# Kernel tuning notes

Measured on AMD Instinct MI355X. Metric: run time of the kernel, lower is better.

Reference implementation:

```python
import jax, jax.numpy as jnp
import numpy as np
from jax import lax

B, C, D, H, W = 2, 1, 128, 128, 128
CONSCIOUSNESS_WEIGHT = 0.1


def _field(depth, height, width, dtype):
    # sin(2*pi*(d+h+w)/(D+H+W)) broadcast over batch/channel
    d = jnp.arange(depth, dtype=dtype)[:, None, None]
    h = jnp.arange(height, dtype=dtype)[None, :, None]
    w = jnp.arange(width, dtype=dtype)[None, None, :]
    phase = 2.0 * jnp.pi * (d + h + w) / (depth + height + width)
    return jnp.sin(phase)  # [D,H,W]


def _conv3d(x, w, b):
    y = lax.conv_general_dilated(
        x, w, window_strides=(1, 1, 1), padding='SAME',
        dimension_numbers=('NCDHW', 'OIDHW', 'NCDHW'))
    return y + b[None, :, None, None, None]


def setup_inputs() -> dict:
    key = jax.random.key(0)
    ks = jax.random.split(key, 4)
    fan1 = 1 * 27
    fan2 = 8 * 27
    fan3 = 16 * 27
    return {
        'cube_data': jax.random.normal(ks[0], (B, C, D, H, W), dtype=jnp.float32),
        'w1': jax.random.normal(ks[1], (8, 1, 3, 3, 3), dtype=jnp.float32) / np.sqrt(fan1),
        'b1': jnp.zeros((8,), dtype=jnp.float32),
        'w2': jax.random.normal(ks[2], (16, 8, 3, 3, 3), dtype=jnp.float32) / np.sqrt(fan2),
        'b2': jnp.zeros((16,), dtype=jnp.float32),
        'w3': jax.random.normal(ks[3], (1, 16, 3, 3, 3), dtype=jnp.float32) / np.sqrt(fan3),
        'b3': jnp.zeros((1,), dtype=jnp.float32),
    }


def reference(cube_data, w1, b1, w2, b2, w3, b3):
    _, _, d, h, w = cube_data.shape
    field = _field(d, h, w, cube_data.dtype)[None, None]  # [1,1,D,H,W]
    integrated = cube_data * (1.0 + CONSCIOUSNESS_WEIGHT * field)
    x = jax.nn.relu(_conv3d(integrated, w1, b1))
    x = jax.nn.relu(_conv3d(x, w2, b2))
    x = jnp.tanh(_conv3d(x, w3, b3))
    return x
```

## Files before the change

### kernel.cpp

```cpp
#include <hip/hip_runtime.h>
#include <hip/hip_fp16.h>

#define VOX (128 * 128 * 128)
#define P 130
#define PP (P * P)
#define PVOX (P * P * P)
#define LROW 130
#define PLANE (6 * LROW)
#define C3PLANE 1560

typedef unsigned short u16;
typedef _Float16 f16x2 __attribute__((ext_vector_type(2)));
typedef _Float16 f16x8 __attribute__((ext_vector_type(8)));
typedef __attribute__((ext_vector_type(4))) float f32x4;

__device__ __forceinline__ u16 f2h(float f) {
    return __builtin_bit_cast(unsigned short, (_Float16)f);
}
__device__ __forceinline__ unsigned pkh_relu(float a, float b) {
    float ra = a > 0.f ? a : 0.f, rb = b > 0.f ? b : 0.f;
    return (unsigned)f2h(ra) | ((unsigned)f2h(rb) << 16);
}
__device__ __forceinline__ f16x2 h2(unsigned u) { return __builtin_bit_cast(f16x2, u); }

__device__ __forceinline__ float dot2(unsigned a, unsigned b, float c) {
#if __has_builtin(__builtin_amdgcn_fdot2)
    return __builtin_amdgcn_fdot2(h2(a), h2(b), c, false);
#else
    f16x2 av = h2(a), bv = h2(b);
    c = fmaf((float)av.x, (float)bv.x, c);
    return fmaf((float)av.y, (float)bv.y, c);
#endif
}

__device__ __forceinline__ float fast_tanh(float x) {
    float e = __expf(2.0f * x);
    return 1.0f - 2.0f * __builtin_amdgcn_rcpf(1.0f + e);
}

__device__ __forceinline__ void gload_lds16(const u16* g, u16* l) {
    __builtin_amdgcn_global_load_lds(
        (const __attribute__((address_space(1))) unsigned int*)g,
        (__attribute__((address_space(3))) unsigned int*)l,
        16, 0, 0);
}

__global__ __launch_bounds__(256) void integrate_kernel(
    const float* __restrict__ in, u16* __restrict__ x0,
    const float* __restrict__ w1, const float* __restrict__ w2,
    const float* __restrict__ w3, u16* __restrict__ w2frag,
    unsigned* __restrict__ w3p, float* __restrict__ w1c,
    u16* __restrict__ x1, u16* __restrict__ x2) {
    int i = blockIdx.x * 256 + threadIdx.x;
    if (i < 3584) {
        int j = i & 7, l = (i >> 3) & 63, s = i >> 9;
        int tap = s * 4 + (l >> 4), oc = l & 15;
        float v = (tap < 27) ? w2[(oc * 8 + j) * 27 + tap] : 0.0f;
        w2frag[i] = f2h(v);
    }
    if (i < 216) {
        int tap = i >> 3, j = i & 7;
        w3p[i] = (unsigned)f2h(w3[(2 * j) * 27 + tap]) |
                 ((unsigned)f2h(w3[(2 * j + 1) * 27 + tap]) << 16);
        int c = i & 7;
        w1c[i] = w1[c * 27 + tap];
    }
    if (i >= PVOX) return;
    int d = i / PP;
    int r = i - d * PP;
    int h = r / P;
    int w = r - h * P;
    const bool interior = (d >= 1 && d <= 128 && h >= 1 && h <= 128 && w >= 1 && w <= 128);
    float v = 0.0f;
    if (interior) {
        int s = (d - 1) + (h - 1) + (w - 1);
        float fld = 1.0f + 0.1f * __sinf(6.283185307179586f * (float)s / 384.0f);
        v = in[(size_t)(d - 1) * 16384 + (h - 1) * 128 + (w - 1)] * fld;
    } else {
        uint4 z = {0u, 0u, 0u, 0u};
        *(uint4*)(x1 + (size_t)i * 8) = z;
        *(uint4*)(x2 + (size_t)i * 16) = z;
        *(uint4*)(x2 + (size_t)i * 16 + 8) = z;
    }
    x0[i] = f2h(v);
}

__global__ __launch_bounds__(256) void integrate_light_kernel(
    const float* __restrict__ in, u16* __restrict__ x0) {
    const int i = blockIdx.x * 256 + threadIdx.x;
    const int d = i >> 14, h = (i >> 7) & 127, w = i & 127;
    const int s = d + h + w;
    const float fld = 1.0f + 0.1f * __sinf((float)s * 0.016362461737446838f);
    x0[(size_t)(d + 1) * PP + (h + 1) * P + (w + 1)] = f2h(in[i] * fld);
}

__global__ __launch_bounds__(256) void conv1_kernel(
    const u16* __restrict__ x0, const float* __restrict__ w1c,
    const float* __restrict__ b1, u16* __restrict__ x1) {
    const int t = blockIdx.x * 256 + threadIdx.x;
    const int w0 = (t & 63) * 2;
    const int h0 = ((t >> 6) & 31) * 4;
    const int d = t >> 11;

    float acc[4][2][8];
#pragma unroll
    for (int c = 0; c < 8; ++c) {
        const float b = b1[c];
#pragma unroll
        for (int i = 0; i < 4; ++i) { acc[i][0][c] = b; acc[i][1][c] = b; }
    }

#pragma unroll
    for (int dz = 0; dz < 3; ++dz) {
        const u16* zb = x0 + (size_t)(d + dz) * PP + (size_t)h0 * P + w0;
        const float* wz = w1c + dz * 9 * 8;
#pragma unroll
        for (int r = 0; r < 6; ++r) {
            const u16* rp = zb + r * P;
            const unsigned u0 = *(const unsigned*)rp;
            const unsigned u1 = *(const unsigned*)(rp + 2);
            float vv[4];
            vv[0] = (float)h2(u0).x; vv[1] = (float)h2(u0).y;
            vv[2] = (float)h2(u1).x; vv[3] = (float)h2(u1).y;
#pragma unroll
            for (int dy = 0; dy < 3; ++dy) {
                const int i = r - dy;
                if (i < 0 || i > 3) continue;
#pragma unroll
                for (int dx = 0; dx < 3; ++dx) {
                    const float a0 = vv[dx];
                    const float a1 = vv[dx + 1];
                    const float* wp = wz + (dy * 3 + dx) * 8;
#pragma unroll
                    for (int c = 0; c < 8; ++c) {
                        const float wt = wp[c];
                        acc[i][0][c] = fmaf(wt, a0, acc[i][0][c]);
                        acc[i][1][c] = fmaf(wt, a1, acc[i][1][c]);
                    }
                }
            }
        }
    }
    const size_t e0 = ((size_t)(d + 1) * P + (h0 + 1)) * P + (w0 + 1);
#pragma unroll
    for (int i = 0; i < 4; ++i) {
        uint4 oA, oB;
        oA.x = pkh_relu(acc[i][0][0], acc[i][0][1]);
        oA.y = pkh_relu(acc[i][0][2], acc[i][0][3]);
        oA.z = pkh_relu(acc[i][0][4], acc[i][0][5]);
        oA.w = pkh_relu(acc[i][0][6], acc[i][0][7]);
        oB.x = pkh_relu(acc[i][1][0], acc[i][1][1]);
        oB.y = pkh_relu(acc[i][1][2], acc[i][1][3]);
        oB.z = pkh_relu(acc[i][1][4], acc[i][1][5]);
        oB.w = pkh_relu(acc[i][1][6], acc[i][1][7]);
        *(uint4*)(x1 + (e0 + (size_t)i * P) * 8) = oA;
        *(uint4*)(x1 + (e0 + (size_t)i * P + 1) * 8) = oB;
    }
}

__global__ __launch_bounds__(256) void conv2_mfma_kernel(
    const u16* __restrict__ x1, const u16* __restrict__ w2frag,
    const float* __restrict__ b2, u16* __restrict__ x2) {
    __shared__ u16 sm[4 * PLANE * 8];

    const int tid = threadIdx.x;
    const int lane = tid & 63;
    const int wv = tid >> 6;
    const int q = lane >> 4;
    const int mi = lane & 15;
    const int D0 = (blockIdx.x >> 5) * 8;
    const int h0 = (blockIdx.x & 31) * 4;

    f16x8 wf[7];
#pragma unroll
    for (int s = 0; s < 7; ++s)
        wf[s] = *(const f16x8*)(w2frag + (size_t)(s * 64 + lane) * 8);

#pragma unroll
    for (int p = 0; p < 3; ++p) {
        const int pd = D0 + p;
        const int slot = pd & 3;
        const u16* gb = x1 + ((size_t)(pd * P + h0) * P) * 8;
        u16* lb = sm + (size_t)slot * PLANE * 8;
#pragma unroll
        for (int k = 0; k < 3; ++k) {
            const int u0 = wv * 64 + k * 256;
            gload_lds16(gb + (size_t)(u0 + lane) * 8, lb + (size_t)u0 * 8);
        }
        if (wv == 0 && lane < PLANE - 768)
            gload_lds16(gb + (size_t)(768 + lane) * 8, lb + (size_t)768 * 8);
    }
    __syncthreads();

    const float4 bv = *(const float4*)(b2 + q * 4);

#pragma unroll 1
    for (int i = 0; i < 8; ++i) {
        const int dout = D0 + i;

        if (i < 7) {
            const int pd = dout + 3;
            const int slot = pd & 3;
            const u16* gb = x1 + ((size_t)(pd * P + h0) * P) * 8;
            u16* lb = sm + (size_t)slot * PLANE * 8;
#pragma unroll
            for (int k = 0; k < 3; ++k) {
                const int u0 = wv * 64 + k * 256;
                gload_lds16(gb + (size_t)(u0 + lane) * 8, lb + (size_t)u0 * 8);
            }
            if (wv == 0 && lane < PLANE - 768)
                gload_lds16(gb + (size_t)(768 + lane) * 8, lb + (size_t)768 * 8);
        }

        f32x4 acc[8];
#pragma unroll
        for (int t = 0; t < 8; ++t) acc[t] = (f32x4){0.f, 0.f, 0.f, 0.f};

#pragma unroll
        for (int s = 0; s < 7; ++s) {
            int tap = s * 4 + q;
            if (tap > 26) tap = 26;
            const int dz = tap / 9;
            const int rem = tap - dz * 9;
            const int dy = rem / 3;
            const int dx = rem - dy * 3;
            const int slot = (dout + dz) & 3;
            const u16* bp = sm + ((size_t)(slot * 6 + wv + dy) * LROW + (mi + dx)) * 8;
#pragma unroll
            for (int t = 0; t < 8; ++t) {
                f16x8 act = *(const f16x8*)(bp + t * 128);
                acc[t] = __builtin_amdgcn_mfma_f32_16x16x32_f16(wf[s], act, acc[t], 0, 0, 0);
            }
        }

        const size_t obase = ((size_t)(dout + 1) * P + (h0 + wv + 1)) * P + 1;
#pragma unroll
        for (int t = 0; t < 8; ++t) {
            uint2 o;
            o.x = pkh_relu(acc[t][0] + bv.x, acc[t][1] + bv.y);
            o.y = pkh_relu(acc[t][2] + bv.z, acc[t][3] + bv.w);
            *(uint2*)(x2 + (obase + 16 * t + mi) * 16 + q * 4) = o;
        }

        if (i < 7) __syncthreads();
    }
}

__global__ __launch_bounds__(256, 1) void conv3_kernel(
    const u16* __restrict__ x2, const unsigned* __restrict__ w3p,
    const float* __restrict__ b3, float* __restrict__ out) {
    __shared__ u16 sm[4 * C3PLANE * 8];

    const int tid = threadIdx.x;
    const int lane = tid & 63;
    const int wv = tid >> 6;
    const int half = tid & 1;
    const int p = tid >> 1;
    const int D0 = (blockIdx.x >> 5) * 8;
    const int h0 = (blockIdx.x & 31) * 4;

    uint4 wt[27];
#pragma unroll
    for (int q = 0; q < 27; ++q)
        wt[q] = *(const uint4*)(w3p + q * 8 + half * 4);

#pragma unroll
    for (int pp = 0; pp < 3; ++pp) {
        const int pd = D0 + pp;
        const int slot = pd & 3;
        const u16* gb = x2 + ((size_t)(pd * P + h0) * P) * 16;
        u16* lb = sm + (size_t)slot * C3PLANE * 8;
#pragma unroll
        for (int k = 0; k < 6; ++k) {
            const int u0 = wv * 64 + k * 256;
            gload_lds16(gb + (size_t)(u0 + lane) * 8, lb + (size_t)u0 * 8);
        }
        if (wv == 0 && lane < C3PLANE - 1536)
            gload_lds16(gb + (size_t)(1536 + lane) * 8, lb + (size_t)1536 * 8);
    }
    __syncthreads();

    const float bias = b3[0];

#pragma unroll 1
    for (int i = 0; i < 8; ++i) {
        const int dout = D0 + i;

        if (i < 7) {
            const int pd = dout + 3;
            const int slot = pd & 3;
            const u16* gb = x2 + ((size_t)(pd * P + h0) * P) * 16;
            u16* lb = sm + (size_t)slot * C3PLANE * 8;
#pragma unroll
            for (int k = 0; k < 6; ++k) {
                const int u0 = wv * 64 + k * 256;
                gload_lds16(gb + (size_t)(u0 + lane) * 8, lb + (size_t)u0 * 8);
            }
            if (wv == 0 && lane < C3PLANE - 1536)
                gload_lds16(gb + (size_t)(1536 + lane) * 8, lb + (size_t)1536 * 8);
        }

        float acc[4] = {0.f, 0.f, 0.f, 0.f};
#pragma unroll
        for (int dz = 0; dz < 3; ++dz) {
            const int slot = (dout + dz) & 3;
            const u16* sp = sm + (size_t)slot * C3PLANE * 8 + (size_t)half * 8;
#pragma unroll
            for (int r = 0; r < 6; ++r) {
                const u16* rp = sp + (size_t)(r * 130 + p) * 16;
                const uint4 v0 = *(const uint4*)(rp);
                const uint4 v1 = *(const uint4*)(rp + 16);
                const uint4 v2 = *(const uint4*)(rp + 32);
#pragma unroll
                for (int dy = 0; dy < 3; ++dy) {
                    const int ii = r - dy;
                    if (ii < 0 || ii > 3) continue;
#pragma unroll
                    for (int dx = 0; dx < 3; ++dx) {
                        const uint4 wq = wt[dz * 9 + dy * 3 + dx];
                        const uint4 v = (dx == 0) ? v0 : ((dx == 1) ? v1 : v2);
                        float a = acc[ii];
                        a = dot2(v.x, wq.x, a);
                        a = dot2(v.y, wq.y, a);
                        a = dot2(v.z, wq.z, a);
                        a = dot2(v.w, wq.w, a);
                        acc[ii] = a;
                    }
                }
            }
        }

#pragma unroll
        for (int k = 0; k < 4; ++k) acc[k] += __shfl_xor(acc[k], 1);

        const size_t ob = ((size_t)dout * 128 + h0) * 128 + p;
#pragma unroll
        for (int k = 0; k < 2; ++k) {
            const int hr = half * 2 + k;
            out[ob + (size_t)hr * 128] = fast_tanh(acc[hr] + bias);
        }

        if (i < 7) __syncthreads();
    }
}

extern "C" void kernel_launch(void* const* d_in, const int* in_sizes, int n_in,
                              void* d_out, int out_size, void* d_ws, size_t ws_size,
                              hipStream_t stream) {
    const float* cube = (const float*)d_in[0];
    const float* w1 = (const float*)d_in[1];
    const float* b1 = (const float*)d_in[2];
    const float* w2 = (const float*)d_in[3];
    const float* b2 = (const float*)d_in[4];
    const float* w3 = (const float*)d_in[5];
    const float* b3 = (const float*)d_in[6];
    float* out = (float*)d_out;

    char* ws = (char*)d_ws;
    u16* w2frag = (u16*)ws;
    unsigned* w3p = (unsigned*)(ws + 7168);
    float* w1c = (float*)(ws + 8032);
    u16* x0 = (u16*)(ws + 16384);
    u16* x1 = (u16*)(ws + 16384 + (size_t)PVOX * sizeof(u16));
    u16* x2 = (u16*)(ws + 16384 + (size_t)PVOX * sizeof(u16) + (size_t)PVOX * 8 * sizeof(u16));

    for (int b = 0; b < 2; ++b) {
        if (b == 0) {
            integrate_kernel<<<dim3((PVOX + 255) / 256), dim3(256), 0, stream>>>(
                cube, x0, w1, w2, w3, w2frag, w3p, w1c, x1, x2);
        } else {
            integrate_light_kernel<<<dim3(VOX / 256), dim3(256), 0, stream>>>(
                cube + (size_t)VOX, x0);
        }
        conv1_kernel<<<dim3(VOX / 8 / 256), dim3(256), 0, stream>>>(x0, w1c, b1, x1);
        conv2_mfma_kernel<<<dim3(512), dim3(256), 0, stream>>>(x1, w2frag, b2, x2);
        conv3_kernel<<<dim3(512), dim3(256), 0, stream>>>(
            x2, w3p, b3, out + (size_t)b * VOX);
    }
}
```

Baseline: 234.9 us.

## Split conv3 channels four ways with 512-thread blocks over 16 depth slices

Conv3 now uses 512-thread blocks, and each thread handles 4 of the 16 input channels for one output column instead of 8. The four partial sums are combined with two xor shuffles. Each block walks 16 output depth planes instead of 8, so half as many blocks are launched and the two-plane halo prefetch is amortised over more planes. The intent is more threads per block to hide LDS and global latency, at the cost of extra shuffles and possibly worse load balance across the CUs.

```diff
diff --git a/kernel.cpp b/kernel.cpp
--- a/kernel.cpp
+++ b/kernel.cpp
@@ -246,7 +246,7 @@
     }
 }
 
-__global__ __launch_bounds__(256, 1) void conv3_kernel(
+__global__ __launch_bounds__(512, 1) void conv3_kernel(
     const u16* __restrict__ x2, const unsigned* __restrict__ w3p,
     const float* __restrict__ b3, float* __restrict__ out) {
     __shared__ u16 sm[4 * C3PLANE * 8];
@@ -254,15 +254,15 @@
     const int tid = threadIdx.x;
     const int lane = tid & 63;
     const int wv = tid >> 6;
-    const int half = tid & 1;
-    const int p = tid >> 1;
-    const int D0 = (blockIdx.x >> 5) * 8;
+    const int cq = tid & 3;
+    const int p = tid >> 2;
+    const int D0 = (blockIdx.x >> 5) * 16;
     const int h0 = (blockIdx.x & 31) * 4;
 
-    uint4 wt[27];
+    uint2 wt[27];
 #pragma unroll
     for (int q = 0; q < 27; ++q)
-        wt[q] = *(const uint4*)(w3p + q * 8 + half * 4);
+        wt[q] = *(const uint2*)(w3p + q * 8 + cq * 2);
 
 #pragma unroll
     for (int pp = 0; pp < 3; ++pp) {
@@ -271,8 +271,8 @@
         const u16* gb = x2 + ((size_t)(pd * P + h0) * P) * 16;
         u16* lb = sm + (size_t)slot * C3PLANE * 8;
 #pragma unroll
-        for (int k = 0; k < 6; ++k) {
-            const int u0 = wv * 64 + k * 256;
+        for (int k = 0; k < 3; ++k) {
+            const int u0 = wv * 64 + k * 512;
             gload_lds16(gb + (size_t)(u0 + lane) * 8, lb + (size_t)u0 * 8);
         }
         if (wv == 0 && lane < C3PLANE - 1536)
@@ -283,17 +283,17 @@
     const float bias = b3[0];
 
 #pragma unroll 1
-    for (int i = 0; i < 8; ++i) {
+    for (int i = 0; i < 16; ++i) {
         const int dout = D0 + i;
 
-        if (i < 7) {
+        if (i < 15) {
             const int pd = dout + 3;
             const int slot = pd & 3;
             const u16* gb = x2 + ((size_t)(pd * P + h0) * P) * 16;
             u16* lb = sm + (size_t)slot * C3PLANE * 8;
 #pragma unroll
-            for (int k = 0; k < 6; ++k) {
-                const int u0 = wv * 64 + k * 256;
+            for (int k = 0; k < 3; ++k) {
+                const int u0 = wv * 64 + k * 512;
                 gload_lds16(gb + (size_t)(u0 + lane) * 8, lb + (size_t)u0 * 8);
             }
             if (wv == 0 && lane < C3PLANE - 1536)
@@ -304,43 +304,40 @@
 #pragma unroll
         for (int dz = 0; dz < 3; ++dz) {
             const int slot = (dout + dz) & 3;
-            const u16* sp = sm + (size_t)slot * C3PLANE * 8 + (size_t)half * 8;
+            const u16* sp = sm + (size_t)slot * C3PLANE * 8 + (size_t)cq * 4;
 #pragma unroll
             for (int r = 0; r < 6; ++r) {
                 const u16* rp = sp + (size_t)(r * 130 + p) * 16;
-                const uint4 v0 = *(const uint4*)(rp);
-                const uint4 v1 = *(const uint4*)(rp + 16);
-                const uint4 v2 = *(const uint4*)(rp + 32);
+                const uint2 v0 = *(const uint2*)(rp);
+                const uint2 v1 = *(const uint2*)(rp + 16);
+                const uint2 v2 = *(const uint2*)(rp + 32);
 #pragma unroll
                 for (int dy = 0; dy < 3; ++dy) {
                     const int ii = r - dy;
                     if (ii < 0 || ii > 3) continue;
-#pragma unroll
-                    for (int dx = 0; dx < 3; ++dx) {
-                        const uint4 wq = wt[dz * 9 + dy * 3 + dx];
-                        const uint4 v = (dx == 0) ? v0 : ((dx == 1) ? v1 : v2);
-                        float a = acc[ii];
-                        a = dot2(v.x, wq.x, a);
-                        a = dot2(v.y, wq.y, a);
-                        a = dot2(v.z, wq.z, a);
-                        a = dot2(v.w, wq.w, a);
-                        acc[ii] = a;
-                    }
+                    const uint2 wq0 = wt[dz * 9 + dy * 3 + 0];
+                    const uint2 wq1 = wt[dz * 9 + dy * 3 + 1];
+                    const uint2 wq2 = wt[dz * 9 + dy * 3 + 2];
+                    float a = acc[ii];
+                    a = dot2(v0.x, wq0.x, a);
+                    a = dot2(v0.y, wq0.y, a);
+                    a = dot2(v1.x, wq1.x, a);
+                    a = dot2(v1.y, wq1.y, a);
+                    a = dot2(v2.x, wq2.x, a);
+                    a = dot2(v2.y, wq2.y, a);
+                    acc[ii] = a;
                 }
             }
         }
 
 #pragma unroll
-        for (int k = 0; k < 4; ++k) acc[k] += __shfl_xor(acc[k], 1);
-
-        const size_t ob = ((size_t)dout * 128 + h0) * 128 + p;
-#pragma unroll
-        for (int k = 0; k < 2; ++k) {
-            const int hr = half * 2 + k;
-            out[ob + (size_t)hr * 128] = fast_tanh(acc[hr] + bias);
-        }
-
-        if (i < 7) __syncthreads();
+        for (int k = 0; k < 4; ++k) {
+            acc[k] += __shfl_xor(acc[k], 1);
+            acc[k] += __shfl_xor(acc[k], 2);
+        }
+        out[((size_t)dout * 128 + h0 + cq) * 128 + p] = fast_tanh(acc[cq] + bias);
+
+        if (i < 15) __syncthreads();
     }
 }
 
@@ -374,7 +371,7 @@
         }
         conv1_kernel<<<dim3(VOX / 8 / 256), dim3(256), 0, stream>>>(x0, w1c, b1, x1);
         conv2_mfma_kernel<<<dim3(512), dim3(256), 0, stream>>>(x1, w2frag, b2, x2);
-        conv3_kernel<<<dim3(512), dim3(256), 0, stream>>>(
+        conv3_kernel<<<dim3(256), dim3(512), 0, stream>>>(
             x2, w3p, b3, out + (size_t)b * VOX);
     }
 }
```

Result: faster. 228.9 us (-2.6%).
